# Kernel tuning notes

Measured on AMD Instinct MI355X. Metric: run time of the kernel, lower is better.

## Reference

```python
import jax, jax.numpy as jnp
import numpy as np

N_NODES = 100000
N_EDGES = 50000
NNZ = 1600000
C = 128
EPS = 0.0  # train_eps=False -> fixed buffer


def setup_inputs() -> dict:
    key = jax.random.key(0)
    k0, k1, k2, k3, k4 = jax.random.split(key, 5)
    x_0 = jax.random.normal(k0, (N_NODES, C), dtype=jnp.float32)
    node_idx = jax.random.randint(k1, (NNZ,), 0, N_NODES, dtype=jnp.int64)
    edge_idx = jax.random.randint(k2, (NNZ,), 0, N_EDGES, dtype=jnp.int64)
    # Linear(in_channels, in_channels) params (kaiming-uniform-ish scale)
    lim = 1.0 / np.sqrt(C)
    W = jax.random.uniform(k3, (C, C), minval=-lim, maxval=lim, dtype=jnp.float32)
    b = jax.random.uniform(k4, (C,), minval=-lim, maxval=lim, dtype=jnp.float32)
    return {"x_0": x_0, "node_idx": node_idx, "edge_idx": edge_idx, "W": W, "b": b}


def reference(x_0, node_idx, edge_idx, W, b):
    # Step 1: x_1 = B_1^T @ x_0  (hyperedge e sums features of its nodes)
    x_1 = jax.ops.segment_sum(x_0[node_idx], edge_idx, num_segments=N_EDGES)
    # Step 2: m_{1->0} = B_1 @ x_1 (node sums features of its incident hyperedges)
    m_1_0 = jax.ops.segment_sum(x_1[edge_idx], node_idx, num_segments=N_NODES)
    # Step 3: GIN update: Theta @ ((1+eps)*x_0 + m)
    out_0 = ((1.0 + EPS) * x_0 + m_1_0) @ W.T + b
    return (out_0, x_1)
```

## Files before the change

kernel.cpp:

```cpp
#include <hip/hip_runtime.h>
#include <stdint.h>

#define N_NODES 100000
#define N_EDGES 50000
#define C 128
#define NB 196
#define CAP 12288

typedef short short8 __attribute__((ext_vector_type(8)));
typedef float f32x4  __attribute__((ext_vector_type(4)));

__device__ __forceinline__ unsigned int bf16rne(float f) {
    unsigned int u = __float_as_uint(f);
    return (u + 0x7FFFu + ((u >> 16) & 1u)) >> 16;
}
__device__ __forceinline__ unsigned int pk_bf16(float x, float y) {
    return (bf16rne(y) << 16) | bf16rne(x);
}
__device__ __forceinline__ float bf_lo(unsigned int u) { return __uint_as_float(u << 16); }
__device__ __forceinline__ float bf_hi(unsigned int u) { return __uint_as_float(u & 0xFFFF0000u); }

__global__ __launch_bounds__(256) void conv_bf16(
    const float2* __restrict__ in, unsigned int* __restrict__ outp, int n2)
{
    int i = blockIdx.x * 256 + threadIdx.x;
    if (i < n2) { float2 v = in[i]; outp[i] = pk_bf16(v.x, v.y); }
}

__global__ __launch_bounds__(256) void coarse_hist(
    const int* __restrict__ nidx, const int* __restrict__ eidx,
    int* __restrict__ Ceh, int* __restrict__ Cnh, int nnz)
{
    __shared__ int he[NB], hn[NB];
    int t = threadIdx.x;
    int chunk0 = blockIdx.x * 4096;
    for (int k = t; k < NB; k += 256) { he[k] = 0; hn[k] = 0; }
    __syncthreads();
#pragma unroll 4
    for (int j = 0; j < 16; ++j) {
        int i = chunk0 + j * 256 + t;
        if (i < nnz) {
            atomicAdd(&he[eidx[i] >> 8], 1);
            atomicAdd(&hn[nidx[i] >> 9], 1);
        }
    }
    __syncthreads();
    for (int k = t; k < NB; k += 256) {
        if (he[k]) atomicAdd(&Ceh[k], he[k]);
        if (hn[k]) atomicAdd(&Cnh[k], hn[k]);
    }
}

__global__ __launch_bounds__(256) void coarse_scan(
    const int* __restrict__ Ceh, const int* __restrict__ Cnh,
    int* __restrict__ Cecur, int* __restrict__ Cncur)
{
    __shared__ int s[256];
    int t = threadIdx.x;
    int v = (t < NB) ? Ceh[t] : 0;
    s[t] = v; __syncthreads();
    for (int d = 1; d < 256; d <<= 1) {
        int u = (t >= d) ? s[t - d] : 0;
        __syncthreads(); s[t] += u; __syncthreads();
    }
    if (t < NB) Cecur[t] = s[t] - v;
    __syncthreads();
    v = (t < NB) ? Cnh[t] : 0;
    s[t] = v; __syncthreads();
    for (int d = 1; d < 256; d <<= 1) {
        int u = (t >= d) ? s[t - d] : 0;
        __syncthreads(); s[t] += u; __syncthreads();
    }
    if (t < NB) Cncur[t] = s[t] - v;
}

__global__ __launch_bounds__(256) void partition_kernel(
    const int* __restrict__ nidx, const int* __restrict__ eidx,
    int* __restrict__ Cecur, int* __restrict__ Cncur,
    uint64_t* __restrict__ pe, uint64_t* __restrict__ pn, int nnz)
{
    __shared__ int he[NB], hn[NB], be[NB], bn[NB];
    int t = threadIdx.x;
    int chunk0 = blockIdx.x * 4096;
    for (int k = t; k < NB; k += 256) { he[k] = 0; hn[k] = 0; }
    __syncthreads();
#pragma unroll 4
    for (int j = 0; j < 16; ++j) {
        int i = chunk0 + j * 256 + t;
        if (i < nnz) {
            atomicAdd(&he[eidx[i] >> 8], 1);
            atomicAdd(&hn[nidx[i] >> 9], 1);
        }
    }
    __syncthreads();
    for (int k = t; k < NB; k += 256) {
        be[k] = atomicAdd(&Cecur[k], he[k]);
        bn[k] = atomicAdd(&Cncur[k], hn[k]);
        he[k] = 0; hn[k] = 0;
    }
    __syncthreads();
#pragma unroll 4
    for (int j = 0; j < 16; ++j) {
        int i = chunk0 + j * 256 + t;
        if (i < nnz) {
            int e = eidx[i], n = nidx[i];
            int re = atomicAdd(&he[e >> 8], 1);
            pe[be[e >> 8] + re] = ((uint64_t)e << 32) | (uint32_t)n;
            int rn = atomicAdd(&hn[n >> 9], 1);
            pn[bn[n >> 9] + rn] = ((uint64_t)n << 32) | (uint32_t)e;
        }
    }
}

__global__ __launch_bounds__(256) void bucket_scatter_ex(
    const uint64_t* __restrict__ pe, const uint64_t* __restrict__ pn,
    const int* __restrict__ Cecur, const int* __restrict__ Cncur,
    int* __restrict__ e_list, int* __restrict__ n_list,
    int* __restrict__ eoff, int* __restrict__ noff)
{
    __shared__ int cnt[512], cur[512], s[256];
    __shared__ int vals[CAP];
    bool eside = blockIdx.x < NB;
    int b = eside ? blockIdx.x : blockIdx.x - NB;
    const uint64_t* pairs = eside ? pe : pn;
    const int* endarr     = eside ? Cecur : Cncur;
    int* out              = eside ? e_list : n_list;
    int* off              = eside ? eoff : noff;
    int kpb   = eside ? 256 : 512;
    int nkeys = eside ? N_EDGES : N_NODES;
    int key0 = b * kpb;
    int nk = nkeys - key0; if (nk > kpb) nk = kpb;
    if (nk <= 0) return;
    int start = (b == 0) ? 0 : endarr[b - 1];
    int end   = endarr[b];
    int t = threadIdx.x;

    for (int k = t; k < nk; k += 256) cnt[k] = 0;
    __syncthreads();
    for (int i = start + t; i < end; i += 256)
        atomicAdd(&cnt[(int)(pairs[i] >> 32) - key0], 1);
    __syncthreads();
    int k0 = 2 * t, k1 = 2 * t + 1;
    int c0 = (k0 < nk) ? cnt[k0] : 0;
    int c1 = (k1 < nk) ? cnt[k1] : 0;
    int local = c0 + c1;
    s[t] = local; __syncthreads();
    for (int d = 1; d < 256; d <<= 1) {
        int u = (t >= d) ? s[t - d] : 0;
        __syncthreads(); s[t] += u; __syncthreads();
    }
    int excl = s[t] - local;
    if (k0 < nk) { cur[k0] = excl;      off[key0 + k0] = start + excl; }
    if (k1 < nk) { cur[k1] = excl + c0; off[key0 + k1] = start + excl + c0; }
    if (b == NB - 1 && t == 0) off[nkeys] = end;
    __syncthreads();
    for (int i = start + t; i < end; i += 256) {
        uint64_t p = pairs[i];
        int key = (int)(p >> 32) - key0;
        int val = (int)(uint32_t)p;
        int pos = atomicAdd(&cur[key], 1);
        if (pos < CAP) vals[pos] = val;
        else out[start + pos] = val;
    }
    __syncthreads();
    int sz = end - start; if (sz > CAP) sz = CAP;
    for (int j = t; j < sz; j += 256) out[start + j] = vals[j];
}

__device__ __forceinline__ float2 gather_bf16_rows(
    const unsigned int* __restrict__ src, const int* __restrict__ list,
    int s0, int s1, int lane)
{
    float ax0=0,ay0=0,ax1=0,ay1=0,ax2=0,ay2=0,ax3=0,ay3=0;
    float ax4=0,ay4=0,ax5=0,ay5=0,ax6=0,ay6=0,ax7=0,ay7=0;
    for (int base = s0; base < s1; base += 64) {
        int cnt = s1 - base; if (cnt > 64) cnt = 64;
        int my = (lane < cnt) ? list[base + lane] : 0;
        int j = 0;
        for (; j + 8 <= cnt; j += 8) {
            int g0 = __shfl(my, j+0), g1 = __shfl(my, j+1);
            int g2 = __shfl(my, j+2), g3 = __shfl(my, j+3);
            int g4 = __shfl(my, j+4), g5 = __shfl(my, j+5);
            int g6 = __shfl(my, j+6), g7 = __shfl(my, j+7);
            unsigned int u0 = src[(size_t)g0 * 64 + lane];
            unsigned int u1 = src[(size_t)g1 * 64 + lane];
            unsigned int u2 = src[(size_t)g2 * 64 + lane];
            unsigned int u3 = src[(size_t)g3 * 64 + lane];
            unsigned int u4 = src[(size_t)g4 * 64 + lane];
            unsigned int u5 = src[(size_t)g5 * 64 + lane];
            unsigned int u6 = src[(size_t)g6 * 64 + lane];
            unsigned int u7 = src[(size_t)g7 * 64 + lane];
            ax0 += bf_lo(u0); ay0 += bf_hi(u0);  ax1 += bf_lo(u1); ay1 += bf_hi(u1);
            ax2 += bf_lo(u2); ay2 += bf_hi(u2);  ax3 += bf_lo(u3); ay3 += bf_hi(u3);
            ax4 += bf_lo(u4); ay4 += bf_hi(u4);  ax5 += bf_lo(u5); ay5 += bf_hi(u5);
            ax6 += bf_lo(u6); ay6 += bf_hi(u6);  ax7 += bf_lo(u7); ay7 += bf_hi(u7);
        }
        for (; j < cnt; ++j) {
            int g = __shfl(my, j);
            unsigned int u = src[(size_t)g * 64 + lane];
            ax0 += bf_lo(u); ay0 += bf_hi(u);
        }
    }
    ax0+=ax1; ay0+=ay1; ax2+=ax3; ay2+=ay3; ax4+=ax5; ay4+=ay5; ax6+=ax7; ay6+=ay7;
    ax0+=ax2; ay0+=ay2; ax4+=ax6; ay4+=ay6;
    ax0+=ax4; ay0+=ay4;
    return make_float2(ax0, ay0);
}

__global__ __launch_bounds__(256) void seg_sum(
    const unsigned int* __restrict__ x0h, const int* __restrict__ list,
    const int* __restrict__ off, float2* __restrict__ x1,
    unsigned int* __restrict__ x1h, int nseg)
{
    int wid  = (blockIdx.x * 256 + threadIdx.x) >> 6;
    int lane = threadIdx.x & 63;
    if (wid >= nseg) return;
    float2 acc = gather_bf16_rows(x0h, list, off[wid], off[wid + 1], lane);
    x1 [(size_t)wid * 64 + lane] = acc;
    x1h[(size_t)wid * 64 + lane] = pk_bf16(acc.x, acc.y);
}

__global__ __launch_bounds__(256) void gin_fused(
    const float2* __restrict__ x0, const unsigned int* __restrict__ x1h,
    const int* __restrict__ n_list, const int* __restrict__ noff,
    const unsigned short* __restrict__ Wh, const float* __restrict__ b,
    float* __restrict__ out)
{
    __shared__ __align__(16) unsigned short ins[32][136];
    int t = threadIdx.x;
    int lane = t & 63, w = t >> 6;
    int row0 = blockIdx.x * 32;

    for (int r = w * 8; r < w * 8 + 8; ++r) {
        int node = row0 + r;
        float2 base = x0[(size_t)node * 64 + lane];
        float2 g = gather_bf16_rows(x1h, n_list, noff[node], noff[node + 1], lane);
        *(unsigned int*)&ins[r][lane * 2] = pk_bf16(base.x + g.x, base.y + g.y);
    }
    __syncthreads();

    int mt  = w & 1;
    int ntb = (w >> 1) * 4;
    int l15  = lane & 15;
    int koff = (lane >> 4) * 8;
    int arow = mt * 16 + l15;

    f32x4 acc0 = {0,0,0,0}, acc1 = {0,0,0,0}, acc2 = {0,0,0,0}, acc3 = {0,0,0,0};
#pragma unroll
    for (int kt = 0; kt < C; kt += 32) {
        short8 a = *(const short8*)&ins[arow][kt + koff];
        short8 b0 = *(const short8*)&Wh[(size_t)((ntb + 0) * 16 + l15) * C + kt + koff];
        short8 b1 = *(const short8*)&Wh[(size_t)((ntb + 1) * 16 + l15) * C + kt + koff];
        short8 b2 = *(const short8*)&Wh[(size_t)((ntb + 2) * 16 + l15) * C + kt + koff];
        short8 b3 = *(const short8*)&Wh[(size_t)((ntb + 3) * 16 + l15) * C + kt + koff];
        acc0 = __builtin_amdgcn_mfma_f32_16x16x32_bf16(a, b0, acc0, 0, 0, 0);
        acc1 = __builtin_amdgcn_mfma_f32_16x16x32_bf16(a, b1, acc1, 0, 0, 0);
        acc2 = __builtin_amdgcn_mfma_f32_16x16x32_bf16(a, b2, acc2, 0, 0, 0);
        acc3 = __builtin_amdgcn_mfma_f32_16x16x32_bf16(a, b3, acc3, 0, 0, 0);
    }

    int drow = row0 + mt * 16 + (lane >> 4) * 4;
#pragma unroll
    for (int n = 0; n < 4; ++n) {
        f32x4 accv = (n == 0) ? acc0 : (n == 1) ? acc1 : (n == 2) ? acc2 : acc3;
        int colg = (ntb + n) * 16 + l15;
        float bias = b[colg];
#pragma unroll
        for (int j = 0; j < 4; ++j)
            out[(size_t)(drow + j) * C + colg] = accv[j] + bias;
    }
}

__global__ __launch_bounds__(256) void scatter_rows(
    const float4* __restrict__ src, const int* __restrict__ gather_idx,
    const int* __restrict__ scatter_idx, float* __restrict__ dst, int nnz)
{
    int gid = blockIdx.x * 256 + threadIdx.x;
    int row = gid >> 5, lane = gid & 31;
    if (row >= nnz) return;
    float4 v = src[(size_t)gather_idx[row] * 32 + lane];
    float* d = dst + (size_t)scatter_idx[row] * C + lane * 4;
    atomicAdd(d + 0, v.x); atomicAdd(d + 1, v.y);
    atomicAdd(d + 2, v.z); atomicAdd(d + 3, v.w);
}

__global__ __launch_bounds__(256) void gin_gemm(
    const float* __restrict__ x0, const float* __restrict__ m,
    const float* __restrict__ W, const float* __restrict__ b,
    float* __restrict__ out)
{
    __shared__ float Ws[32][129];
    __shared__ float insf[32][33];
    int t = threadIdx.x;
    int col = t & 127, rg = t >> 7;
    int row0 = blockIdx.x * 32;
    float acc[16];
#pragma unroll
    for (int r = 0; r < 16; ++r) acc[r] = 0.f;
    float bias = b[col];
    for (int kt = 0; kt < C; kt += 32) {
#pragma unroll
        for (int j = 0; j < 16; ++j) {
            int i = j * 256 + t, wc = i >> 5, kl = i & 31;
            Ws[kl][wc] = W[(size_t)wc * C + kt + kl];
        }
#pragma unroll
        for (int j = 0; j < 4; ++j) {
            int i = j * 256 + t, r = i >> 5, kl = i & 31;
            size_t gi = (size_t)(row0 + r) * C + kt + kl;
            insf[r][kl] = x0[gi] + m[gi];
        }
        __syncthreads();
#pragma unroll
        for (int kl = 0; kl < 32; ++kl) {
            float wv = Ws[kl][col];
#pragma unroll
            for (int r = 0; r < 16; ++r)
                acc[r] += insf[rg * 16 + r][kl] * wv;
        }
        __syncthreads();
    }
#pragma unroll
    for (int r = 0; r < 16; ++r)
        out[(size_t)(row0 + rg * 16 + r) * C + col] = acc[r] + bias;
}

extern "C" void kernel_launch(void* const* d_in, const int* in_sizes, int n_in,
                              void* d_out, int out_size, void* d_ws, size_t ws_size,
                              hipStream_t stream) {
    const float* x0 = (const float*)d_in[0];
    const int* nidx = (const int*)d_in[1];
    const int* eidx = (const int*)d_in[2];
    const float* W  = (const float*)d_in[3];
    const float* b  = (const float*)d_in[4];

    float* out0 = (float*)d_out;
    float* x1   = out0 + (size_t)N_NODES * C;
    int nnz = in_sizes[1];

    auto align64 = [](char* q) {
        return (char*)(((uintptr_t)q + 63) & ~(uintptr_t)63);
    };
    char* p = (char*)d_ws;
    uint64_t* pe = (uint64_t*)p;
    uint64_t* pn = pe + nnz;
    unsigned int* x0h = (unsigned int*)pe;
    p = align64((char*)(pn + nnz));
    int* e_list = (int*)p; p = align64(p + (size_t)nnz * 4);
    int* n_list = (int*)p; p = align64(p + (size_t)nnz * 4);
    int* eoff   = (int*)p; p = align64(p + (size_t)(N_EDGES + 1) * 4);
    int* noff   = (int*)p; p = align64(p + (size_t)(N_NODES + 1) * 4);
    int* Ceh    = (int*)p;
    int* Cnh    = Ceh + NB;
    p = align64((char*)(Cnh + NB));
    int* Cecur  = (int*)p; p = align64(p + NB * 4);
    int* Cncur  = (int*)p; p = align64(p + NB * 4);
    unsigned int* x1h = (unsigned int*)p; p = align64(p + (size_t)N_EDGES * 64 * 4);
    unsigned int* Whu = (unsigned int*)p; p = align64(p + (size_t)C * C / 2 * 4);
    size_t needed = (size_t)(p - (char*)d_ws);

    if (ws_size < needed) {
        float* m = (float*)d_ws;
        hipMemsetAsync(x1, 0, (size_t)N_EDGES * C * sizeof(float), stream);
        hipMemsetAsync(m,  0, (size_t)N_NODES * C * sizeof(float), stream);
        int blocks = (nnz + 7) / 8;
        scatter_rows<<<blocks, 256, 0, stream>>>((const float4*)x0, nidx, eidx, x1, nnz);
        scatter_rows<<<blocks, 256, 0, stream>>>((const float4*)x1, eidx, nidx, m, nnz);
        gin_gemm<<<N_NODES / 32, 256, 0, stream>>>(x0, m, W, b, out0);
        return;
    }

    int pblocks = (nnz + 4095) / 4096;

    hipMemsetAsync(Ceh, 0, 2 * NB * sizeof(int), stream);
    coarse_hist<<<pblocks, 256, 0, stream>>>(nidx, eidx, Ceh, Cnh, nnz);
    coarse_scan<<<1, 256, 0, stream>>>(Ceh, Cnh, Cecur, Cncur);
    partition_kernel<<<pblocks, 256, 0, stream>>>(
        nidx, eidx, Cecur, Cncur, pe, pn, nnz);
    bucket_scatter_ex<<<2 * NB, 256, 0, stream>>>(
        pe, pn, Cecur, Cncur, e_list, n_list, eoff, noff);

    conv_bf16<<<(N_NODES * 64 + 255) / 256, 256, 0, stream>>>(
        (const float2*)x0, x0h, N_NODES * 64);
    conv_bf16<<<(C * C / 2 + 255) / 256, 256, 0, stream>>>(
        (const float2*)W, Whu, C * C / 2);

    seg_sum<<<(N_EDGES * 64 + 255) / 256, 256, 0, stream>>>(
        x0h, e_list, eoff, (float2*)x1, x1h, N_EDGES);

    gin_fused<<<N_NODES / 32, 256, 0, stream>>>(
        (const float2*)x0, x1h, n_list, noff,
        (const unsigned short*)Whu, b, out0);
}
```

Before: 263.3 us.

## Pack partition pairs into 32-bit words, merge conversions, read bf16 x0 in GIN

Partition pairs are now packed into 32-bit words holding the local bucket key and the value, instead of 64-bit pairs. This halves the scatter and read traffic in partition and bucket_scatter. The two bf16 conversion kernels and the histogram memset are merged into one launch, and x0h gets its own buffer so it no longer aliases the pair storage. gin_fused reads the bf16 x0 instead of fp32 x0, which cuts bandwidth but adds a small precision loss on the residual term.

```diff
diff --git a/kernel.cpp b/kernel.cpp
--- a/kernel.cpp
+++ b/kernel.cpp
@@ -6,6 +6,7 @@
 #define C 128
 #define NB 196
 #define CAP 12288
+#define X0_BLOCKS 25000
 
 typedef short short8 __attribute__((ext_vector_type(8)));
 typedef float f32x4  __attribute__((ext_vector_type(4)));
@@ -20,11 +21,23 @@
 __device__ __forceinline__ float bf_lo(unsigned int u) { return __uint_as_float(u << 16); }
 __device__ __forceinline__ float bf_hi(unsigned int u) { return __uint_as_float(u & 0xFFFF0000u); }
 
-__global__ __launch_bounds__(256) void conv_bf16(
-    const float2* __restrict__ in, unsigned int* __restrict__ outp, int n2)
-{
-    int i = blockIdx.x * 256 + threadIdx.x;
-    if (i < n2) { float2 v = in[i]; outp[i] = pk_bf16(v.x, v.y); }
+__global__ __launch_bounds__(256) void conv_all(
+    const float2* __restrict__ x0, const float2* __restrict__ W,
+    unsigned int* __restrict__ x0h, unsigned int* __restrict__ Whu,
+    int* __restrict__ CehCnh)
+{
+    int bid = blockIdx.x, t = threadIdx.x;
+    if (bid < X0_BLOCKS) {
+        int i = bid * 256 + t;
+        float2 v = x0[i];
+        x0h[i] = pk_bf16(v.x, v.y);
+        if (bid == 0)
+            for (int k = t; k < 2 * NB; k += 256) CehCnh[k] = 0;
+    } else {
+        int i = (bid - X0_BLOCKS) * 256 + t;
+        float2 v = W[i];
+        Whu[i] = pk_bf16(v.x, v.y);
+    }
 }
 
 __global__ __launch_bounds__(256) void coarse_hist(
@@ -77,7 +90,7 @@
 __global__ __launch_bounds__(256) void partition_kernel(
     const int* __restrict__ nidx, const int* __restrict__ eidx,
     int* __restrict__ Cecur, int* __restrict__ Cncur,
-    uint64_t* __restrict__ pe, uint64_t* __restrict__ pn, int nnz)
+    unsigned int* __restrict__ pe, unsigned int* __restrict__ pn, int nnz)
 {
     __shared__ int he[NB], hn[NB], be[NB], bn[NB];
     int t = threadIdx.x;
@@ -105,15 +118,15 @@
         if (i < nnz) {
             int e = eidx[i], n = nidx[i];
             int re = atomicAdd(&he[e >> 8], 1);
-            pe[be[e >> 8] + re] = ((uint64_t)e << 32) | (uint32_t)n;
+            pe[be[e >> 8] + re] = (unsigned int)((e & 255) | (n << 8));
             int rn = atomicAdd(&hn[n >> 9], 1);
-            pn[bn[n >> 9] + rn] = ((uint64_t)n << 32) | (uint32_t)e;
+            pn[bn[n >> 9] + rn] = (unsigned int)((n & 511) | (e << 9));
         }
     }
 }
 
 __global__ __launch_bounds__(256) void bucket_scatter_ex(
-    const uint64_t* __restrict__ pe, const uint64_t* __restrict__ pn,
+    const unsigned int* __restrict__ pe, const unsigned int* __restrict__ pn,
     const int* __restrict__ Cecur, const int* __restrict__ Cncur,
     int* __restrict__ e_list, int* __restrict__ n_list,
     int* __restrict__ eoff, int* __restrict__ noff)
@@ -122,11 +135,13 @@
     __shared__ int vals[CAP];
     bool eside = blockIdx.x < NB;
     int b = eside ? blockIdx.x : blockIdx.x - NB;
-    const uint64_t* pairs = eside ? pe : pn;
-    const int* endarr     = eside ? Cecur : Cncur;
-    int* out              = eside ? e_list : n_list;
-    int* off              = eside ? eoff : noff;
-    int kpb   = eside ? 256 : 512;
+    const unsigned int* pairs = eside ? pe : pn;
+    const int* endarr         = eside ? Cecur : Cncur;
+    int* out                  = eside ? e_list : n_list;
+    int* off                  = eside ? eoff : noff;
+    int shift = eside ? 8 : 9;
+    int mask  = (1 << shift) - 1;
+    int kpb   = 1 << shift;
     int nkeys = eside ? N_EDGES : N_NODES;
     int key0 = b * kpb;
     int nk = nkeys - key0; if (nk > kpb) nk = kpb;
@@ -138,7 +153,7 @@
     for (int k = t; k < nk; k += 256) cnt[k] = 0;
     __syncthreads();
     for (int i = start + t; i < end; i += 256)
-        atomicAdd(&cnt[(int)(pairs[i] >> 32) - key0], 1);
+        atomicAdd(&cnt[(int)(pairs[i] & mask)], 1);
     __syncthreads();
     int k0 = 2 * t, k1 = 2 * t + 1;
     int c0 = (k0 < nk) ? cnt[k0] : 0;
@@ -155,9 +170,9 @@
     if (b == NB - 1 && t == 0) off[nkeys] = end;
     __syncthreads();
     for (int i = start + t; i < end; i += 256) {
-        uint64_t p = pairs[i];
-        int key = (int)(p >> 32) - key0;
-        int val = (int)(uint32_t)p;
+        unsigned int p = pairs[i];
+        int key = (int)(p & mask);
+        int val = (int)(p >> shift);
         int pos = atomicAdd(&cur[key], 1);
         if (pos < CAP) vals[pos] = val;
         else out[start + pos] = val;
@@ -221,7 +236,7 @@
 }
 
 __global__ __launch_bounds__(256) void gin_fused(
-    const float2* __restrict__ x0, const unsigned int* __restrict__ x1h,
+    const unsigned int* __restrict__ x0h, const unsigned int* __restrict__ x1h,
     const int* __restrict__ n_list, const int* __restrict__ noff,
     const unsigned short* __restrict__ Wh, const float* __restrict__ b,
     float* __restrict__ out)
@@ -233,9 +248,10 @@
 
     for (int r = w * 8; r < w * 8 + 8; ++r) {
         int node = row0 + r;
-        float2 base = x0[(size_t)node * 64 + lane];
+        unsigned int bu = x0h[(size_t)node * 64 + lane];
         float2 g = gather_bf16_rows(x1h, n_list, noff[node], noff[node + 1], lane);
-        *(unsigned int*)&ins[r][lane * 2] = pk_bf16(base.x + g.x, base.y + g.y);
+        g.x += bf_lo(bu); g.y += bf_hi(bu);
+        *(unsigned int*)&ins[r][lane * 2] = pk_bf16(g.x, g.y);
     }
     __syncthreads();
 
@@ -342,10 +358,9 @@
         return (char*)(((uintptr_t)q + 63) & ~(uintptr_t)63);
     };
     char* p = (char*)d_ws;
-    uint64_t* pe = (uint64_t*)p;
-    uint64_t* pn = pe + nnz;
-    unsigned int* x0h = (unsigned int*)pe;
-    p = align64((char*)(pn + nnz));
+    unsigned int* pe = (unsigned int*)p; p = align64(p + (size_t)nnz * 4);
+    unsigned int* pn = (unsigned int*)p; p = align64(p + (size_t)nnz * 4);
+    unsigned int* x0h = (unsigned int*)p; p = align64(p + (size_t)N_NODES * 64 * 4);
     int* e_list = (int*)p; p = align64(p + (size_t)nnz * 4);
     int* n_list = (int*)p; p = align64(p + (size_t)nnz * 4);
     int* eoff   = (int*)p; p = align64(p + (size_t)(N_EDGES + 1) * 4);
@@ -372,7 +387,9 @@
 
     int pblocks = (nnz + 4095) / 4096;
 
-    hipMemsetAsync(Ceh, 0, 2 * NB * sizeof(int), stream);
+    conv_all<<<X0_BLOCKS + C * C / 2 / 256, 256, 0, stream>>>(
+        (const float2*)x0, (const float2*)W, x0h, Whu, Ceh);
+
     coarse_hist<<<pblocks, 256, 0, stream>>>(nidx, eidx, Ceh, Cnh, nnz);
     coarse_scan<<<1, 256, 0, stream>>>(Ceh, Cnh, Cecur, Cncur);
     partition_kernel<<<pblocks, 256, 0, stream>>>(
@@ -380,15 +397,10 @@
     bucket_scatter_ex<<<2 * NB, 256, 0, stream>>>(
         pe, pn, Cecur, Cncur, e_list, n_list, eoff, noff);
 
-    conv_bf16<<<(N_NODES * 64 + 255) / 256, 256, 0, stream>>>(
-        (const float2*)x0, x0h, N_NODES * 64);
-    conv_bf16<<<(C * C / 2 + 255) / 256, 256, 0, stream>>>(
-        (const float2*)W, Whu, C * C / 2);
-
     seg_sum<<<(N_EDGES * 64 + 255) / 256, 256, 0, stream>>>(
         x0h, e_list, eoff, (float2*)x1, x1h, N_EDGES);
 
     gin_fused<<<N_NODES / 32, 256, 0, stream>>>(
-        (const float2*)x0, x1h, n_list, noff,
+        x0h, x1h, n_list, noff,
         (const unsigned short*)Whu, b, out0);
 }
```

Measured after the change: 248.5 us. 1.06x faster.
